# Optimization experiments

Hardware: AMD Instinct MI355X
Metric: run time of the kernel (lower is better)

The kernel has to match this reference:

```python
import jax, jax.numpy as jnp
import numpy as np
from jax import lax

INT8_NARROW = (-127.0, 127.0)   # brevitas Int8WeightPerTensorFloat (narrow range)
INT8_FULL = (-128.0, 127.0)     # brevitas Int8ActPerTensorFloat
INT32 = (-2.0**31, 2.0**31 - 1)


def _fake_quant(v, scale, qmin, qmax):
    # round-to-nearest, clip, dequant (per-tensor)
    return jnp.clip(jnp.round(v / scale), qmin, qmax) * scale


def _conv(x, w, stride):
    return lax.conv_general_dilated(
        x, w, window_strides=(stride, stride), padding=[(1, 1), (1, 1)],
        dimension_numbers=("NCHW", "OIHW", "NCHW"))


def setup_inputs() -> dict:
    key = jax.random.key(0)
    ks = jax.random.split(key, 5)
    B, Cin, Cout, H = 64, 256, 512, 28
    x = jax.random.normal(ks[0], (B, Cin, H, H), dtype=jnp.float32)
    w1 = jax.random.normal(ks[1], (Cout, Cin, 3, 3), dtype=jnp.float32) * 0.05
    b1 = jax.random.normal(ks[2], (Cout,), dtype=jnp.float32) * 0.01
    w2 = jax.random.normal(ks[3], (Cout, Cout, 3, 3), dtype=jnp.float32) * 0.05
    b2 = jax.random.normal(ks[4], (Cout,), dtype=jnp.float32) * 0.01
    return {
        "x": x, "w1": w1, "b1": b1, "w2": w2, "b2": b2,
        "in_scale": jnp.full((1,), 0.05, dtype=jnp.float32),
        "act1_scale": jnp.full((1,), 0.05, dtype=jnp.float32),
        "act2_scale": jnp.full((1,), 0.05, dtype=jnp.float32),
    }


def reference(x, w1, b1, w2, b2, in_scale, act1_scale, act2_scale):
    s_in = in_scale[0]
    s_a1 = act1_scale[0]
    s_a2 = act2_scale[0]

    # conv1: per-tensor int8 weight fake-quant (max-abs stats, narrow range)
    s_w1 = jnp.max(jnp.abs(w1)) / 127.0
    wq1 = _fake_quant(w1, s_w1, *INT8_NARROW)
    bq1 = _fake_quant(b1, s_in * s_w1, *INT32)  # Int32Bias: scale = in_scale*w_scale
    out = _conv(x, wq1, 2) + bq1[None, :, None, None]

    # act1: int8 activation fake-quant (learned per-tensor scale)
    out = _fake_quant(out, s_a1, *INT8_FULL)

    # conv2
    s_w2 = jnp.max(jnp.abs(w2)) / 127.0
    wq2 = _fake_quant(w2, s_w2, *INT8_NARROW)
    bq2 = _fake_quant(b2, s_a1 * s_w2, *INT32)
    out = _conv(out, wq2, 1) + bq2[None, :, None, None]

    # act2
    out = _fake_quant(out, s_a2, *INT8_FULL)
    return out
```

## Files before the change

### kernel.cpp

```cpp
#include <hip/hip_runtime.h>

typedef int i32x4 __attribute__((ext_vector_type(4)));

__device__ __forceinline__ void gl_lds16(const signed char* g, signed char* l) {
    __builtin_amdgcn_global_load_lds(
        (const __attribute__((address_space(1))) void*)g,
        (__attribute__((address_space(3))) void*)l, 16, 0, 0);
}

#define XQ_SCALE 2048.0f
#define XQ_DELTA (1.0f / 2048.0f)

__global__ __launch_bounds__(256) void absmax2_kernel(const float* __restrict__ w1,
                                                      const float* __restrict__ w2,
                                                      float* __restrict__ part) {
    __shared__ float sred[4];
    const bool second = blockIdx.x >= 256;
    const float* w = second ? w2 : w1;
    const int n4 = second ? 589824 : 294912;
    float m = 0.0f;
    for (int i = (blockIdx.x & 255) * 256 + threadIdx.x; i < n4; i += 65536) {
        float4 v = ((const float4*)w)[i];
        m = fmaxf(m, fmaxf(fmaxf(fabsf(v.x), fabsf(v.y)), fmaxf(fabsf(v.z), fabsf(v.w))));
    }
#pragma unroll
    for (int off = 32; off > 0; off >>= 1)
        m = fmaxf(m, __shfl_down(m, off));
    if ((threadIdx.x & 63) == 0) sred[threadIdx.x >> 6] = m;
    __syncthreads();
    if (threadIdx.x == 0)
        part[blockIdx.x] = fmaxf(fmaxf(sred[0], sred[1]), fmaxf(sred[2], sred[3]));
}

__device__ __forceinline__ float block_max256(const float* __restrict__ part, int base,
                                              float* __restrict__ sred) {
    float m = part[base + (threadIdx.x & 255)];
#pragma unroll
    for (int off = 32; off > 0; off >>= 1)
        m = fmaxf(m, __shfl_down(m, off));
    __syncthreads();
    if ((threadIdx.x & 63) == 0) sred[threadIdx.x >> 6] = m;
    __syncthreads();
    return fmaxf(fmaxf(sred[0], sred[1]), fmaxf(sred[2], sred[3]));
}

__global__ __launch_bounds__(256) void prep_all_kernel(
    const float* __restrict__ x,
    const float* __restrict__ w1, const float* __restrict__ w2,
    const float* __restrict__ b1, const float* __restrict__ b2,
    const float* __restrict__ part,
    const float* __restrict__ in_scale, const float* __restrict__ act1_scale,
    signed char* __restrict__ wq1, signed char* __restrict__ wq2,
    float* __restrict__ bq1, float* __restrict__ bq2,
    float* __restrict__ wmax,
    signed char* __restrict__ xhi, signed char* __restrict__ xlo,
    signed char* __restrict__ act) {
    __shared__ __align__(16) signed char sw[4608];
    __shared__ float t[128][33];
    __shared__ float sred[4];
    const int blk = blockIdx.x;
    const int tid = threadIdx.x;
    const uint4 z = {0, 0, 0, 0};

    if (blk < 512) {
        const float inv_s = 127.0f / block_max256(part, 0, sred);
        const int n = blk;
#pragma unroll
        for (int rd = 0; rd < 9; ++rd) {
            const int idx = rd * 256 + tid;
            const float v = w1[n * 2304 + idx];
            float q = rintf(v * inv_s);
            q = fminf(fmaxf(q, -127.0f), 127.0f);
            const int cin = idx / 9;
            const int r = idx - cin * 9;
            sw[r * 256 + cin] = (signed char)(int)q;
        }
        __syncthreads();
        if (tid < 144) *(uint4*)&wq1[n * 2304 + tid * 16] = *(const uint4*)&sw[tid * 16];
    } else if (blk < 1024) {
        const float inv_s = 127.0f / block_max256(part, 256, sred);
        const int n = blk - 512;
#pragma unroll
        for (int rd = 0; rd < 18; ++rd) {
            const int idx = rd * 256 + tid;
            const float v = w2[n * 4608 + idx];
            float q = rintf(v * inv_s);
            q = fminf(fmaxf(q, -127.0f), 127.0f);
            const int cin = idx / 9;
            const int r = idx - cin * 9;
            sw[r * 512 + cin] = (signed char)(int)q;
        }
        __syncthreads();
        for (int o = tid; o < 288; o += 256)
            *(uint4*)&wq2[n * 4608 + o * 16] = *(const uint4*)&sw[o * 16];
    } else if (blk == 1024) {
        const float m1 = block_max256(part, 0, sred);
        const float m2 = block_max256(part, 256, sred);
        if (tid == 0) { wmax[0] = m1; wmax[1] = m2; }
        if (tid < 512) {
            const float s = (*in_scale) * (m1 * (1.0f / 127.0f));
        }
        for (int idx = tid; idx < 1024; idx += 256) {
            if (idx < 512) {
                const float s = (*in_scale) * (m1 * (1.0f / 127.0f));
                float q = rintf(b1[idx] / s);
                q = fminf(fmaxf(q, -2147483648.0f), 2147483648.0f);
                bq1[idx] = q * s;
            } else {
                const int j = idx - 512;
                const float s = (*act1_scale) * (m2 * (1.0f / 127.0f));
                float q = rintf(b2[j] / s);
                q = fminf(fmaxf(q, -2147483648.0f), 2147483648.0f);
                bq2[j] = q * s;
            }
        }
    } else if (blk < 1489) {
        const int thr = (blk - 1025) * 256 + tid;
        const int b = thr / (116 * 16);
        const int rr = thr - b * (116 * 16);
        const int p = rr >> 4;
        const int ch = rr & 15;
        int h, w;
        if (p < 30)      { h = 0;          w = p; }
        else if (p < 60) { h = 29;         w = p - 30; }
        else if (p < 88) { h = p - 60 + 1; w = 0; }
        else             { h = p - 88 + 1; w = 29; }
        const int off = (b * 900 + h * 30 + w) * 256 + ch * 16;
        *(uint4*)(xhi + off) = z;
        *(uint4*)(xlo + off) = z;
    } else if (blk < 1969) {
        const int thr = (blk - 1489) * 256 + tid;
        const int b = thr / (60 * 32);
        const int rr = thr - b * (60 * 32);
        const int p = rr >> 5;
        const int ch = rr & 31;
        int h, w;
        if (p < 16)      { h = 0;          w = p; }
        else if (p < 32) { h = 15;         w = p - 16; }
        else if (p < 46) { h = p - 32 + 1; w = 0; }
        else             { h = p - 46 + 1; w = 15; }
        const int off = (b * 256 + h * 16 + w) * 512 + ch * 16;
        *(uint4*)(act + off) = z;
    } else {
        const int xb = blk - 1969;
        const int hwb = xb % 25;
        const int rest = xb / 25;
        const int cb = rest & 1;
        const int b = rest >> 1;
        const int c0 = cb * 128;
        const int hw0 = hwb * 32;
#pragma unroll
        for (int ci = 0; ci < 16; ++ci) {
            const int crow = (tid >> 5) + ci * 8;
            const int hw = hw0 + (tid & 31);
            float v = 0.0f;
            if (hw < 784) v = x[(b * 256 + c0 + crow) * 784 + hw];
            t[crow][tid & 31] = v;
        }
        __syncthreads();
        const int hw_l = tid >> 3;
        const int cg = (tid & 7) * 16;
        const int hw = hw0 + hw_l;
        if (hw < 784) {
            union { signed char c[16]; uint4 u; } ph, pl;
#pragma unroll
            for (int j = 0; j < 16; ++j) {
                const float v = t[cg + j][hw_l];
                int q = (int)rintf(v * XQ_SCALE);
                q = max(-16383, min(16383, q));
                ph.c[j] = (signed char)(q >> 7);
                pl.c[j] = (signed char)(q & 127);
            }
            const int r = hw / 28;
            const int o = (b * 900 + (r + 1) * 30 + (hw - r * 28) + 1) * 256 + c0 + cg;
            *(uint4*)&xhi[o] = ph.u;
            *(uint4*)&xlo[o] = pl.u;
        }
    }
}

template<int CIN, int STRIDE, int HP, int HOUT, bool SPLIT, bool FINAL>
__global__ __launch_bounds__(128) void conv_gemm_kernel(
    const signed char* __restrict__ Ahi,
    const signed char* __restrict__ Alo,
    const signed char* __restrict__ Wt,
    const float* __restrict__ bias,
    const float* __restrict__ wmax,
    const float* __restrict__ s_pre,
    const float* __restrict__ s_act,
    signed char* __restrict__ act_out,
    float* __restrict__ out_final)
{
    constexpr int K = 9 * CIN;
    constexpr int HW = HOUT * HOUT;
    constexpr int NIT = K / 128;
    constexpr int NC = SPLIT ? 16 : 12;
    constexpr int NACC = SPLIT ? 8 : 4;
    constexpr int BSOFF = SPLIT ? 16384 : 8192;
    constexpr int BUFSZ = BSOFF + 16384;

    __shared__ __align__(16) signed char sm0[BUFSZ];
    __shared__ __align__(16) signed char sm1[BUFSZ];

    const int tid = threadIdx.x;
    const int lane = tid & 63;
    const int wv = tid >> 6;
    const int quad = lane >> 4;
    const int l16 = lane & 15;
    const int m0 = blockIdx.y * 64;
    const int n0 = blockIdx.x * 128;

    const int lrow = lane >> 3;
    const int koff = ((lane & 7) ^ lrow) * 16;

    const signed char* srcb[NC];
    int dsto[NC];
    bool isA[NC];
#pragma unroll
    for (int i = 0; i < NC; ++i) {
        const int g = wv * NC + i;
        int type, c;
        if (SPLIT) {
            type = (g < 8) ? 0 : (g < 16 ? 1 : 2);
            c = (g < 8) ? g : (g < 16 ? g - 8 : g - 16);
        } else {
            type = (g < 8) ? 0 : 2;
            c = (g < 8) ? g : g - 8;
        }
        const int r = c * 8 + lrow;
        if (type == 2) {
            srcb[i] = Wt + (n0 + r) * K + koff;
            dsto[i] = BSOFF + c * 1024;
            isA[i] = false;
        } else {
            const int m = m0 + r;
            const int b = m / HW;
            const int rem = m - b * HW;
            const int oh = rem / HOUT;
            const int ow = rem - oh * HOUT;
            const int off = ((b * HP + oh * STRIDE) * HP + ow * STRIDE) * CIN + koff;
            srcb[i] = (type == 0 ? Ahi : Alo) + off;
            dsto[i] = (type == 0 ? 0 : 8192) + c * 1024;
            isA[i] = true;
        }
    }

    i32x4 acc[NACC][4];
#pragma unroll
    for (int mi = 0; mi < NACC; ++mi)
#pragma unroll
        for (int ni = 0; ni < 4; ++ni)
            acc[mi][ni] = i32x4{0, 0, 0, 0};

    auto stage = [&](int k0, signed char* buf) {
        const int r9 = k0 / CIN;
        const int kh = r9 / 3;
        const int kw = r9 - kh * 3;
        const int ashift = (kh * HP + kw) * CIN + (k0 & (CIN - 1));
#pragma unroll
        for (int i = 0; i < NC; ++i)
            gl_lds16(srcb[i] + (isA[i] ? ashift : k0), buf + dsto[i]);
    };

    auto compute = [&](const signed char* buf) {
#pragma unroll
        for (int ks = 0; ks < 2; ++ks) {
            i32x4 af[NACC];
            i32x4 bfr[4];
#pragma unroll
            for (int mi = 0; mi < 4; ++mi) {
                const int row = mi * 16 + l16;
                const int sl = ((ks * 4 + quad) ^ (row & 7)) * 16;
                af[mi] = *(const i32x4*)&buf[row * 128 + sl];
                if constexpr (SPLIT)
                    af[mi + 4] = *(const i32x4*)&buf[8192 + row * 128 + sl];
            }
#pragma unroll
            for (int ni = 0; ni < 4; ++ni) {
                const int row = wv * 64 + ni * 16 + l16;
                const int sl = ((ks * 4 + quad) ^ (row & 7)) * 16;
                bfr[ni] = *(const i32x4*)&buf[BSOFF + row * 128 + sl];
            }
#pragma unroll
            for (int mi = 0; mi < 4; ++mi)
#pragma unroll
                for (int ni = 0; ni < 4; ++ni) {
                    acc[mi][ni] = __builtin_amdgcn_mfma_i32_16x16x64_i8(af[mi], bfr[ni], acc[mi][ni], 0, 0, 0);
                    if constexpr (SPLIT)
                        acc[mi + 4][ni] = __builtin_amdgcn_mfma_i32_16x16x64_i8(af[mi + 4], bfr[ni], acc[mi + 4][ni], 0, 0, 0);
                }
        }
    };

    stage(0, sm0);
    for (int it = 0; it < NIT; it += 2) {
        __syncthreads();
        stage((it + 1) * 128, sm1);
        compute(sm0);
        __syncthreads();
        if (it + 2 < NIT) stage((it + 2) * 128, sm0);
        compute(sm1);
    }

    float alpha = (*wmax) * (1.0f / 127.0f);
    if (FINAL) alpha *= *s_pre;
    if (SPLIT) alpha *= XQ_DELTA;
    const float sact = *s_act;

    float bv[4];
#pragma unroll
    for (int ni = 0; ni < 4; ++ni)
        bv[ni] = bias[n0 + wv * 64 + ni * 16 + l16];

#pragma unroll
    for (int mi = 0; mi < 4; ++mi) {
#pragma unroll
        for (int i = 0; i < 4; ++i) {
            const int m = m0 + mi * 16 + quad * 4 + i;
            const int b = m / HW;
            const int rem = m - b * HW;
            const int oh = rem / HOUT;
            const int ow = rem - oh * HOUT;
#pragma unroll
            for (int ni = 0; ni < 4; ++ni) {
                const int col = n0 + wv * 64 + ni * 16 + l16;
                int tot = acc[mi][ni][i];
                if constexpr (SPLIT) tot = tot * 128 + acc[mi + 4][ni][i];
                const float v = (float)tot * alpha + bv[ni];
                float q = rintf(v / sact);
                q = fminf(fmaxf(q, -128.0f), 127.0f);
                if (FINAL) {
                    out_final[(b * 512 + col) * HW + oh * HOUT + ow] = q * sact;
                } else {
                    act_out[(b * 256 + (oh + 1) * 16 + (ow + 1)) * 512 + col] = (signed char)(int)q;
                }
            }
        }
    }
}

extern "C" void kernel_launch(void* const* d_in, const int* in_sizes, int n_in,
                              void* d_out, int out_size, void* d_ws, size_t ws_size,
                              hipStream_t stream) {
    const float* x  = (const float*)d_in[0];
    const float* w1 = (const float*)d_in[1];
    const float* b1 = (const float*)d_in[2];
    const float* w2 = (const float*)d_in[3];
    const float* b2 = (const float*)d_in[4];
    const float* in_scale   = (const float*)d_in[5];
    const float* act1_scale = (const float*)d_in[6];
    const float* act2_scale = (const float*)d_in[7];
    float* out = (float*)d_out;

    char* ws = (char*)d_ws;
    float* part = (float*)(ws + 0);
    float* wmax = (float*)(ws + 2048);
    float* bq1 = (float*)(ws + 2176);
    float* bq2 = (float*)(ws + 4224);
    signed char* wq1 = (signed char*)(ws + 8192);
    signed char* wq2 = (signed char*)(ws + 1187840);
    signed char* xhi = (signed char*)(ws + 3547136);
    signed char* xlo = (signed char*)(ws + 18292736);
    signed char* act = (signed char*)(ws + 33038336);

    absmax2_kernel<<<512, 256, 0, stream>>>(w1, w2, part);

    prep_all_kernel<<<5169, 256, 0, stream>>>(
        x, w1, w2, b1, b2, part, in_scale, act1_scale,
        wq1, wq2, bq1, bq2, wmax, xhi, xlo, act);

    conv_gemm_kernel<256, 2, 30, 14, true, false><<<dim3(4, 196), 128, 0, stream>>>(
        xhi, xlo, wq1, bq1, wmax, act1_scale, act1_scale, act, nullptr);

    conv_gemm_kernel<512, 1, 16, 14, false, true><<<dim3(4, 196), 128, 0, stream>>>(
        act, nullptr, wq2, bq2, wmax + 1, act1_scale, act2_scale, nullptr, out);
}
```

Measured before the change: 256.2 us.

## Split conv GEMM work across 4 waves and rebalance preprocessing kernels

The conv GEMM kernel moves from 128 to 256 threads. For the split-precision conv1, the hi and lo activation products go to separate wave pairs. For conv2, K is split between two wave pairs, and the partial accumulators are combined through LDS at the end. The double-buffered prefetch is replaced by a single buffer with a sync on each iteration. The absmax reduction now shares one kernel with the padding and input-quantization work, and weight quantization runs in a separate kernel. This is meant to halve per-wave accumulator pressure and raise occupancy, at the cost of losing load/compute overlap and adding an LDS reduction step.

```diff
diff --git a/kernel.cpp b/kernel.cpp
--- a/kernel.cpp
+++ b/kernel.cpp
@@ -10,27 +10,6 @@
 
 #define XQ_SCALE 2048.0f
 #define XQ_DELTA (1.0f / 2048.0f)
-
-__global__ __launch_bounds__(256) void absmax2_kernel(const float* __restrict__ w1,
-                                                      const float* __restrict__ w2,
-                                                      float* __restrict__ part) {
-    __shared__ float sred[4];
-    const bool second = blockIdx.x >= 256;
-    const float* w = second ? w2 : w1;
-    const int n4 = second ? 589824 : 294912;
-    float m = 0.0f;
-    for (int i = (blockIdx.x & 255) * 256 + threadIdx.x; i < n4; i += 65536) {
-        float4 v = ((const float4*)w)[i];
-        m = fmaxf(m, fmaxf(fmaxf(fabsf(v.x), fabsf(v.y)), fmaxf(fabsf(v.z), fabsf(v.w))));
-    }
-#pragma unroll
-    for (int off = 32; off > 0; off >>= 1)
-        m = fmaxf(m, __shfl_down(m, off));
-    if ((threadIdx.x & 63) == 0) sred[threadIdx.x >> 6] = m;
-    __syncthreads();
-    if (threadIdx.x == 0)
-        part[blockIdx.x] = fmaxf(fmaxf(sred[0], sred[1]), fmaxf(sred[2], sred[3]));
-}
 
 __device__ __forceinline__ float block_max256(const float* __restrict__ part, int base,
                                               float* __restrict__ sred) {
@@ -44,23 +23,111 @@
     return fmaxf(fmaxf(sred[0], sred[1]), fmaxf(sred[2], sred[3]));
 }
 
-__global__ __launch_bounds__(256) void prep_all_kernel(
+__global__ __launch_bounds__(256) void fused_pre_kernel(
     const float* __restrict__ x,
+    const float* __restrict__ w1, const float* __restrict__ w2,
+    float* __restrict__ part,
+    signed char* __restrict__ xhi, signed char* __restrict__ xlo,
+    signed char* __restrict__ act) {
+    __shared__ float t[128][33];
+    __shared__ float sred[4];
+    const int blk = blockIdx.x;
+    const int tid = threadIdx.x;
+    const uint4 z = {0, 0, 0, 0};
+
+    if (blk < 512) {
+        const bool second = blk >= 256;
+        const float* w = second ? w2 : w1;
+        const int n4 = second ? 589824 : 294912;
+        float m = 0.0f;
+        for (int i = (blk & 255) * 256 + tid; i < n4; i += 65536) {
+            float4 v = ((const float4*)w)[i];
+            m = fmaxf(m, fmaxf(fmaxf(fabsf(v.x), fabsf(v.y)), fmaxf(fabsf(v.z), fabsf(v.w))));
+        }
+#pragma unroll
+        for (int off = 32; off > 0; off >>= 1)
+            m = fmaxf(m, __shfl_down(m, off));
+        if ((tid & 63) == 0) sred[tid >> 6] = m;
+        __syncthreads();
+        if (tid == 0)
+            part[blk] = fmaxf(fmaxf(sred[0], sred[1]), fmaxf(sred[2], sred[3]));
+    } else if (blk < 976) {
+        const int thr = (blk - 512) * 256 + tid;
+        const int b = thr / (116 * 16);
+        const int rr = thr - b * (116 * 16);
+        const int p = rr >> 4;
+        const int ch = rr & 15;
+        int h, w;
+        if (p < 30)      { h = 0;          w = p; }
+        else if (p < 60) { h = 29;         w = p - 30; }
+        else if (p < 88) { h = p - 60 + 1; w = 0; }
+        else             { h = p - 88 + 1; w = 29; }
+        const int off = (b * 900 + h * 30 + w) * 256 + ch * 16;
+        *(uint4*)(xhi + off) = z;
+        *(uint4*)(xlo + off) = z;
+    } else if (blk < 1456) {
+        const int thr = (blk - 976) * 256 + tid;
+        const int b = thr / (60 * 32);
+        const int rr = thr - b * (60 * 32);
+        const int p = rr >> 5;
+        const int ch = rr & 31;
+        int h, w;
+        if (p < 16)      { h = 0;          w = p; }
+        else if (p < 32) { h = 15;         w = p - 16; }
+        else if (p < 46) { h = p - 32 + 1; w = 0; }
+        else             { h = p - 46 + 1; w = 15; }
+        const int off = (b * 256 + h * 16 + w) * 512 + ch * 16;
+        *(uint4*)(act + off) = z;
+    } else {
+        const int xb = blk - 1456;
+        const int hwb = xb % 25;
+        const int rest = xb / 25;
+        const int cb = rest & 1;
+        const int b = rest >> 1;
+        const int c0 = cb * 128;
+        const int hw0 = hwb * 32;
+#pragma unroll
+        for (int ci = 0; ci < 16; ++ci) {
+            const int crow = (tid >> 5) + ci * 8;
+            const int hw = hw0 + (tid & 31);
+            float v = 0.0f;
+            if (hw < 784) v = x[(b * 256 + c0 + crow) * 784 + hw];
+            t[crow][tid & 31] = v;
+        }
+        __syncthreads();
+        const int hw_l = tid >> 3;
+        const int cg = (tid & 7) * 16;
+        const int hw = hw0 + hw_l;
+        if (hw < 784) {
+            union { signed char c[16]; uint4 u; } ph, pl;
+#pragma unroll
+            for (int j = 0; j < 16; ++j) {
+                const float v = t[cg + j][hw_l];
+                int q = (int)rintf(v * XQ_SCALE);
+                q = max(-16383, min(16383, q));
+                ph.c[j] = (signed char)(q >> 7);
+                pl.c[j] = (signed char)(q & 127);
+            }
+            const int r = hw / 28;
+            const int o = (b * 900 + (r + 1) * 30 + (hw - r * 28) + 1) * 256 + c0 + cg;
+            *(uint4*)&xhi[o] = ph.u;
+            *(uint4*)&xlo[o] = pl.u;
+        }
+    }
+}
+
+__global__ __launch_bounds__(256) void prep_w_kernel(
     const float* __restrict__ w1, const float* __restrict__ w2,
     const float* __restrict__ b1, const float* __restrict__ b2,
     const float* __restrict__ part,
     const float* __restrict__ in_scale, const float* __restrict__ act1_scale,
     signed char* __restrict__ wq1, signed char* __restrict__ wq2,
     float* __restrict__ bq1, float* __restrict__ bq2,
-    float* __restrict__ wmax,
-    signed char* __restrict__ xhi, signed char* __restrict__ xlo,
-    signed char* __restrict__ act) {
+    float* __restrict__ wmax) {
     __shared__ __align__(16) signed char sw[4608];
-    __shared__ float t[128][33];
     __shared__ float sred[4];
     const int blk = blockIdx.x;
     const int tid = threadIdx.x;
-    const uint4 z = {0, 0, 0, 0};
 
     if (blk < 512) {
         const float inv_s = 127.0f / block_max256(part, 0, sred);
@@ -93,13 +160,10 @@
         __syncthreads();
         for (int o = tid; o < 288; o += 256)
             *(uint4*)&wq2[n * 4608 + o * 16] = *(const uint4*)&sw[o * 16];
-    } else if (blk == 1024) {
+    } else {
         const float m1 = block_max256(part, 0, sred);
         const float m2 = block_max256(part, 256, sred);
         if (tid == 0) { wmax[0] = m1; wmax[1] = m2; }
-        if (tid < 512) {
-            const float s = (*in_scale) * (m1 * (1.0f / 127.0f));
-        }
         for (int idx = tid; idx < 1024; idx += 256) {
             if (idx < 512) {
                 const float s = (*in_scale) * (m1 * (1.0f / 127.0f));
@@ -114,73 +178,11 @@
                 bq2[j] = q * s;
             }
         }
-    } else if (blk < 1489) {
-        const int thr = (blk - 1025) * 256 + tid;
-        const int b = thr / (116 * 16);
-        const int rr = thr - b * (116 * 16);
-        const int p = rr >> 4;
-        const int ch = rr & 15;
-        int h, w;
-        if (p < 30)      { h = 0;          w = p; }
-        else if (p < 60) { h = 29;         w = p - 30; }
-        else if (p < 88) { h = p - 60 + 1; w = 0; }
-        else             { h = p - 88 + 1; w = 29; }
-        const int off = (b * 900 + h * 30 + w) * 256 + ch * 16;
-        *(uint4*)(xhi + off) = z;
-        *(uint4*)(xlo + off) = z;
-    } else if (blk < 1969) {
-        const int thr = (blk - 1489) * 256 + tid;
-        const int b = thr / (60 * 32);
-        const int rr = thr - b * (60 * 32);
-        const int p = rr >> 5;
-        const int ch = rr & 31;
-        int h, w;
-        if (p < 16)      { h = 0;          w = p; }
-        else if (p < 32) { h = 15;         w = p - 16; }
-        else if (p < 46) { h = p - 32 + 1; w = 0; }
-        else             { h = p - 46 + 1; w = 15; }
-        const int off = (b * 256 + h * 16 + w) * 512 + ch * 16;
-        *(uint4*)(act + off) = z;
-    } else {
-        const int xb = blk - 1969;
-        const int hwb = xb % 25;
-        const int rest = xb / 25;
-        const int cb = rest & 1;
-        const int b = rest >> 1;
-        const int c0 = cb * 128;
-        const int hw0 = hwb * 32;
-#pragma unroll
-        for (int ci = 0; ci < 16; ++ci) {
-            const int crow = (tid >> 5) + ci * 8;
-            const int hw = hw0 + (tid & 31);
-            float v = 0.0f;
-            if (hw < 784) v = x[(b * 256 + c0 + crow) * 784 + hw];
-            t[crow][tid & 31] = v;
-        }
-        __syncthreads();
-        const int hw_l = tid >> 3;
-        const int cg = (tid & 7) * 16;
-        const int hw = hw0 + hw_l;
-        if (hw < 784) {
-            union { signed char c[16]; uint4 u; } ph, pl;
-#pragma unroll
-            for (int j = 0; j < 16; ++j) {
-                const float v = t[cg + j][hw_l];
-                int q = (int)rintf(v * XQ_SCALE);
-                q = max(-16383, min(16383, q));
-                ph.c[j] = (signed char)(q >> 7);
-                pl.c[j] = (signed char)(q & 127);
-            }
-            const int r = hw / 28;
-            const int o = (b * 900 + (r + 1) * 30 + (hw - r * 28) + 1) * 256 + c0 + cg;
-            *(uint4*)&xhi[o] = ph.u;
-            *(uint4*)&xlo[o] = pl.u;
-        }
     }
 }
 
 template<int CIN, int STRIDE, int HP, int HOUT, bool SPLIT, bool FINAL>
-__global__ __launch_bounds__(128) void conv_gemm_kernel(
+__global__ __launch_bounds__(256, 3) void conv_gemm_kernel(
     const signed char* __restrict__ Ahi,
     const signed char* __restrict__ Alo,
     const signed char* __restrict__ Wt,
@@ -193,18 +195,17 @@
 {
     constexpr int K = 9 * CIN;
     constexpr int HW = HOUT * HOUT;
-    constexpr int NIT = K / 128;
-    constexpr int NC = SPLIT ? 16 : 12;
-    constexpr int NACC = SPLIT ? 8 : 4;
-    constexpr int BSOFF = SPLIT ? 16384 : 8192;
-    constexpr int BUFSZ = BSOFF + 16384;
-
-    __shared__ __align__(16) signed char sm0[BUFSZ];
-    __shared__ __align__(16) signed char sm1[BUFSZ];
+    constexpr int NIT = SPLIT ? (K / 128) : (K / 256);
+    constexpr int NC = SPLIT ? 8 : 12;
+    constexpr int LDSZ = SPLIT ? 32768 : 49152;
+
+    __shared__ __align__(16) signed char smem[LDSZ];
 
     const int tid = threadIdx.x;
     const int lane = tid & 63;
     const int wv = tid >> 6;
+    const int pair = wv >> 1;
+    const int nh = wv & 1;
     const int quad = lane >> 4;
     const int l16 = lane & 15;
     const int m0 = blockIdx.y * 64;
@@ -213,94 +214,125 @@
     const int lrow = lane >> 3;
     const int koff = ((lane & 7) ^ lrow) * 16;
 
+    const int kbase = SPLIT ? 0 : pair * (K / 2);
+
     const signed char* srcb[NC];
     int dsto[NC];
     bool isA[NC];
-#pragma unroll
-    for (int i = 0; i < NC; ++i) {
-        const int g = wv * NC + i;
-        int type, c;
-        if (SPLIT) {
-            type = (g < 8) ? 0 : (g < 16 ? 1 : 2);
-            c = (g < 8) ? g : (g < 16 ? g - 8 : g - 16);
-        } else {
-            type = (g < 8) ? 0 : 2;
-            c = (g < 8) ? g : g - 8;
-        }
-        const int r = c * 8 + lrow;
-        if (type == 2) {
-            srcb[i] = Wt + (n0 + r) * K + koff;
-            dsto[i] = BSOFF + c * 1024;
-            isA[i] = false;
-        } else {
-            const int m = m0 + r;
-            const int b = m / HW;
-            const int rem = m - b * HW;
-            const int oh = rem / HOUT;
-            const int ow = rem - oh * HOUT;
-            const int off = ((b * HP + oh * STRIDE) * HP + ow * STRIDE) * CIN + koff;
-            srcb[i] = (type == 0 ? Ahi : Alo) + off;
-            dsto[i] = (type == 0 ? 0 : 8192) + c * 1024;
-            isA[i] = true;
-        }
-    }
-
-    i32x4 acc[NACC][4];
-#pragma unroll
-    for (int mi = 0; mi < NACC; ++mi)
+    if constexpr (SPLIT) {
+#pragma unroll
+        for (int i = 0; i < NC; ++i) {
+            const int g = wv * 8 + i;
+            const int type = g >> 3;
+            if (type >= 2) {
+                const int c = g - 16;
+                srcb[i] = Wt + (n0 + c * 8 + lrow) * K + koff;
+                dsto[i] = 16384 + c * 1024;
+                isA[i] = false;
+            } else {
+                const int c = g & 7;
+                const int m = m0 + c * 8 + lrow;
+                const int b = m / HW;
+                const int rem = m - b * HW;
+                const int oh = rem / HOUT;
+                const int ow = rem - oh * HOUT;
+                const int off = ((b * HP + oh * STRIDE) * HP + ow * STRIDE) * CIN + koff;
+                srcb[i] = (type == 0 ? Ahi : Alo) + off;
+                dsto[i] = type * 8192 + c * 1024;
+                isA[i] = true;
+            }
+        }
+    } else {
+#pragma unroll
+        for (int i = 0; i < NC; ++i) {
+            const int g = nh * 12 + i;
+            if (g < 8) {
+                const int c = g;
+                const int m = m0 + c * 8 + lrow;
+                const int b = m / HW;
+                const int rem = m - b * HW;
+                const int oh = rem / HOUT;
+                const int ow = rem - oh * HOUT;
+                const int off = ((b * HP + oh * STRIDE) * HP + ow * STRIDE) * CIN + koff;
+                srcb[i] = Ahi + off;
+                dsto[i] = pair * 24576 + c * 1024;
+                isA[i] = true;
+            } else {
+                const int c = g - 8;
+                srcb[i] = Wt + (n0 + c * 8 + lrow) * K + koff;
+                dsto[i] = pair * 24576 + 8192 + c * 1024;
+                isA[i] = false;
+            }
+        }
+    }
+
+    const int aoff0 = SPLIT ? (pair * 8192) : (pair * 24576);
+    const int boff0 = SPLIT ? 16384 : (pair * 24576 + 8192);
+
+    i32x4 acc[4][4];
+#pragma unroll
+    for (int mi = 0; mi < 4; ++mi)
 #pragma unroll
         for (int ni = 0; ni < 4; ++ni)
             acc[mi][ni] = i32x4{0, 0, 0, 0};
 
-    auto stage = [&](int k0, signed char* buf) {
+    for (int it = 0; it < NIT; ++it) {
+        const int k0 = kbase + it * 128;
         const int r9 = k0 / CIN;
         const int kh = r9 / 3;
         const int kw = r9 - kh * 3;
         const int ashift = (kh * HP + kw) * CIN + (k0 & (CIN - 1));
+
+        __syncthreads();
 #pragma unroll
         for (int i = 0; i < NC; ++i)
-            gl_lds16(srcb[i] + (isA[i] ? ashift : k0), buf + dsto[i]);
-    };
-
-    auto compute = [&](const signed char* buf) {
+            gl_lds16(srcb[i] + (isA[i] ? ashift : k0), &smem[dsto[i]]);
+        __syncthreads();
+
 #pragma unroll
         for (int ks = 0; ks < 2; ++ks) {
-            i32x4 af[NACC];
-            i32x4 bfr[4];
+            i32x4 af[4], bfr[4];
 #pragma unroll
             for (int mi = 0; mi < 4; ++mi) {
                 const int row = mi * 16 + l16;
                 const int sl = ((ks * 4 + quad) ^ (row & 7)) * 16;
-                af[mi] = *(const i32x4*)&buf[row * 128 + sl];
-                if constexpr (SPLIT)
-                    af[mi + 4] = *(const i32x4*)&buf[8192 + row * 128 + sl];
+                af[mi] = *(const i32x4*)&smem[aoff0 + row * 128 + sl];
             }
 #pragma unroll
             for (int ni = 0; ni < 4; ++ni) {
-                const int row = wv * 64 + ni * 16 + l16;
+                const int row = nh * 64 + ni * 16 + l16;
                 const int sl = ((ks * 4 + quad) ^ (row & 7)) * 16;
-                bfr[ni] = *(const i32x4*)&buf[BSOFF + row * 128 + sl];
+                bfr[ni] = *(const i32x4*)&smem[boff0 + row * 128 + sl];
             }
 #pragma unroll
             for (int mi = 0; mi < 4; ++mi)
 #pragma unroll
-                for (int ni = 0; ni < 4; ++ni) {
+                for (int ni = 0; ni < 4; ++ni)
                     acc[mi][ni] = __builtin_amdgcn_mfma_i32_16x16x64_i8(af[mi], bfr[ni], acc[mi][ni], 0, 0, 0);
-                    if constexpr (SPLIT)
-                        acc[mi + 4][ni] = __builtin_amdgcn_mfma_i32_16x16x64_i8(af[mi + 4], bfr[ni], acc[mi + 4][ni], 0, 0, 0);
-                }
-        }
-    };
-
-    stage(0, sm0);
-    for (int it = 0; it < NIT; it += 2) {
-        __syncthreads();
-        stage((it + 1) * 128, sm1);
-        compute(sm0);
-        __syncthreads();
-        if (it + 2 < NIT) stage((it + 2) * 128, sm0);
-        compute(sm1);
-    }
+        }
+    }
+
+    __syncthreads();
+    if (pair == 1) {
+#pragma unroll
+        for (int mi = 0; mi < 4; ++mi)
+#pragma unroll
+            for (int ni = 0; ni < 4; ++ni)
+                *(i32x4*)&smem[nh * 16384 + (mi * 4 + ni) * 1024 + lane * 16] = acc[mi][ni];
+    }
+    __syncthreads();
+    if (pair == 1) return;
+
+#pragma unroll
+    for (int mi = 0; mi < 4; ++mi)
+#pragma unroll
+        for (int ni = 0; ni < 4; ++ni) {
+            const i32x4 other = *(const i32x4*)&smem[nh * 16384 + (mi * 4 + ni) * 1024 + lane * 16];
+            if constexpr (SPLIT)
+                acc[mi][ni] = acc[mi][ni] * 128 + other;
+            else
+                acc[mi][ni] = acc[mi][ni] + other;
+        }
 
     float alpha = (*wmax) * (1.0f / 127.0f);
     if (FINAL) alpha *= *s_pre;
@@ -310,7 +342,7 @@
     float bv[4];
 #pragma unroll
     for (int ni = 0; ni < 4; ++ni)
-        bv[ni] = bias[n0 + wv * 64 + ni * 16 + l16];
+        bv[ni] = bias[n0 + nh * 64 + ni * 16 + l16];
 
 #pragma unroll
     for (int mi = 0; mi < 4; ++mi) {
@@ -323,10 +355,8 @@
             const int ow = rem - oh * HOUT;
 #pragma unroll
             for (int ni = 0; ni < 4; ++ni) {
-                const int col = n0 + wv * 64 + ni * 16 + l16;
-                int tot = acc[mi][ni][i];
-                if constexpr (SPLIT) tot = tot * 128 + acc[mi + 4][ni][i];
-                const float v = (float)tot * alpha + bv[ni];
+                const int col = n0 + nh * 64 + ni * 16 + l16;
+                const float v = (float)acc[mi][ni][i] * alpha + bv[ni];
                 float q = rintf(v / sact);
                 q = fminf(fmaxf(q, -128.0f), 127.0f);
                 if (FINAL) {
@@ -363,15 +393,14 @@
     signed char* xlo = (signed char*)(ws + 18292736);
     signed char* act = (signed char*)(ws + 33038336);
 
-    absmax2_kernel<<<512, 256, 0, stream>>>(w1, w2, part);
-
-    prep_all_kernel<<<5169, 256, 0, stream>>>(
-        x, w1, w2, b1, b2, part, in_scale, act1_scale,
-        wq1, wq2, bq1, bq2, wmax, xhi, xlo, act);
-
-    conv_gemm_kernel<256, 2, 30, 14, true, false><<<dim3(4, 196), 128, 0, stream>>>(
+    fused_pre_kernel<<<4656, 256, 0, stream>>>(x, w1, w2, part, xhi, xlo, act);
+
+    prep_w_kernel<<<1025, 256, 0, stream>>>(w1, w2, b1, b2, part, in_scale, act1_scale,
+                                            wq1, wq2, bq1, bq2, wmax);
+
+    conv_gemm_kernel<256, 2, 30, 14, true, false><<<dim3(4, 196), 256, 0, stream>>>(
         xhi, xlo, wq1, bq1, wmax, act1_scale, act1_scale, act, nullptr);
 
-    conv_gemm_kernel<512, 1, 16, 14, false, true><<<dim3(4, 196), 128, 0, stream>>>(
+    conv_gemm_kernel<512, 1, 16, 14, false, true><<<dim3(4, 196), 256, 0, stream>>>(
         act, nullptr, wq2, bq2, wmax + 1, act1_scale, act2_scale, nullptr, out);
 }
```

New measurement: 247.0 us. 3.6% less time.
